# Optimization experiments

Measured on AMD Instinct MI355X. Metric: run time of the kernel, lower is better.

## Reference

```python
import jax, jax.numpy as jnp
import numpy as np

NUM, K = 5, 3  # grid intervals and spline order, as in KANLayer(num=5, k=3)

def _grid(num=NUM, k=K, lo=-1.0, hi=1.0):
    # base grid: num+1 points on [lo,hi], extended by k knots on each side (pykan extend_grid)
    h = (hi - lo) / num
    return jnp.linspace(lo - k * h, hi + k * h, num + 1 + 2 * k, dtype=jnp.float32)

def b_spline_basis(x, grid, k=K):
    # Cox-de Boor recursion, identical to pykan B_batch. x: (B, In) -> (B, In, num+k)
    xe = x[..., None]
    b = ((xe >= grid[:-1]) & (xe < grid[1:])).astype(x.dtype)  # order-0 indicators
    for d in range(1, k + 1):
        left = (xe - grid[:-(d + 1)]) / (grid[d:-1] - grid[:-(d + 1)])
        right = (grid[d + 1:] - xe) / (grid[d + 1:] - grid[1:-d])
        b = left * b[..., :-1] + right * b[..., 1:]
    return b

def kan_layer(x, coef, sb, ssp, grid):
    # x: (B, In); coef: (Out, In, nb); sb/ssp: (Out, In). mask == 1.
    basis = b_spline_basis(x, grid)                       # (B, In, nb)
    spline = jnp.einsum('big,oig->boi', basis, coef)      # per-edge spline value
    y = sb[None] * jax.nn.silu(x)[:, None, :] + ssp[None] * spline  # (B, Out, In)
    return y.sum(axis=2)                                  # (B, Out)

def setup_inputs() -> dict:
    key = jax.random.key(0)
    ks = jax.random.split(key, 3)
    B, IN, H, OUT, NB = 128, 3072, 256, 10, NUM + K
    return {
        "x": jax.random.normal(ks[0], (B, IN), jnp.float32),
        "coef1": 0.1 * jax.random.normal(ks[1], (H, IN, NB), jnp.float32),
        "scale_base1": jnp.ones((H, IN), jnp.float32),
        "scale_sp1": jnp.ones((H, IN), jnp.float32),
        "coef2": 0.1 * jax.random.normal(ks[2], (OUT, H, NB), jnp.float32),
        "scale_base2": jnp.ones((OUT, H), jnp.float32),
        "scale_sp2": jnp.ones((OUT, H), jnp.float32),
    }

def reference(x, coef1, scale_base1, scale_sp1, coef2, scale_base2, scale_sp2):
    g = _grid()
    h = kan_layer(x, coef1, scale_base1, scale_sp1, g)
    h = jax.nn.selu(h)
    return kan_layer(h, coef2, scale_base2, scale_sp2, g)
```

## Files before the change

kernel.cpp:

```cpp
#include <hip/hip_runtime.h>
#include <hip/hip_bf16.h>
#include <math.h>


#define B_DIM   128
#define IN1     3072
#define OUT1    256
#define NB      8
#define OUT2    10

#define KTOT    27648
#define ROWB    55296
#define SPLITK  108
#define BN      64

typedef short  bf16x8 __attribute__((ext_vector_type(8)));
typedef float  f32x4  __attribute__((ext_vector_type(4)));
typedef unsigned short ushort_t;
typedef unsigned int u32;

__device__ __forceinline__ ushort_t f2bf(float f) {
    union { __hip_bfloat16 h; ushort_t u; } v;
    v.h = __float2bfloat16(f);
    return v.u;
}
__device__ __forceinline__ float bf2f(ushort_t h) {
    union { float f; u32 u; } v; v.u = ((u32)h) << 16;
    return v.f;
}

__device__ __forceinline__ void gl_lds16(const void* g, void* l) {
    __builtin_amdgcn_global_load_lds(
        (const __attribute__((address_space(1))) u32*)g,
        (__attribute__((address_space(3))) u32*)l, 16, 0, 0);
}

__device__ __forceinline__ void basis_silu(float x, float w[8], float& sil) {
    sil = x / (1.0f + __expf(-x));
    float u  = (x + 2.2f) * 2.5f;
    float uf = floorf(u);
    int   j  = (int)uf;
    float t  = u - uf;
    float omt = 1.0f - t;
    float t2 = t * t, t3 = t2 * t;
    float w0 = omt * omt * omt * (1.0f / 6.0f);
    float w1 = (3.0f * t3 - 6.0f * t2 + 4.0f) * (1.0f / 6.0f);
    float w2 = (-3.0f * t3 + 3.0f * t2 + 3.0f * t + 1.0f) * (1.0f / 6.0f);
    float w3 = t3 * (1.0f / 6.0f);
    bool valid = (u >= 0.0f) && (u < 11.0f);
#pragma unroll
    for (int g = 0; g < 8; ++g) {
        int m = g - j + 3;
        float v = (m == 0) ? w0 : (m == 1) ? w1 : (m == 2) ? w2 : (m == 3) ? w3 : 0.0f;
        w[g] = valid ? v : 0.0f;
    }
}

__device__ __forceinline__ float selu_f(float x) {
    const float scale = 1.0507009873554805f;
    const float alpha = 1.6732632423543772f;
    return (x > 0.0f) ? scale * x : scale * alpha * (__expf(x) - 1.0f);
}

__global__ __launch_bounds__(128) void kconv(const float* __restrict__ x,
                                             const float* __restrict__ coef1,
                                             const float* __restrict__ sb1,
                                             const float* __restrict__ ssp1,
                                             char* __restrict__ Ag,
                                             char* __restrict__ Wg) {
    const int blk = blockIdx.x;
    if (blk < 384) {
        const int gid = blk * 128 + threadIdx.x;
        const int b  = gid / 384;
        const int ig = gid - b * 384;
        const int i0 = ig * 8;

        float4 x0 = *reinterpret_cast<const float4*>(x + (size_t)b * IN1 + i0);
        float4 x1 = *reinterpret_cast<const float4*>(x + (size_t)b * IN1 + i0 + 4);
        float xa[8] = {x0.x, x0.y, x0.z, x0.w, x1.x, x1.y, x1.z, x1.w};

        float bs[8][8], sil[8];
#pragma unroll
        for (int p = 0; p < 8; ++p) basis_silu(xa[p], bs[p], sil[p]);

        char* rowp = Ag + (size_t)b * ROWB;
        const int qsw = ((ig & 7) ^ (b & 7)) << 4;
#pragma unroll
        for (int s = 0; s < 9; ++s) {
            ushort_t v[8];
#pragma unroll
            for (int p = 0; p < 8; ++p)
                v[p] = f2bf((s < 8) ? bs[p][s] : sil[p]);
            *reinterpret_cast<uint4*>(rowp + (s * 48 + (ig >> 3)) * 128 + qsw) =
                *reinterpret_cast<const uint4*>(v);
        }
    } else {
        const int gid = (blk - 384) * 128 + threadIdx.x;
        const int o  = gid / 384;
        const int ig = gid - o * 384;
        const int i0 = ig * 8;

        float cf[8][8], sspv[8], sbv[8];
#pragma unroll
        for (int p = 0; p < 8; ++p) {
            const float* cp = coef1 + ((size_t)o * IN1 + i0 + p) * NB;
            float4 c0 = *reinterpret_cast<const float4*>(cp);
            float4 c1 = *reinterpret_cast<const float4*>(cp + 4);
            cf[p][0] = c0.x; cf[p][1] = c0.y; cf[p][2] = c0.z; cf[p][3] = c0.w;
            cf[p][4] = c1.x; cf[p][5] = c1.y; cf[p][6] = c1.z; cf[p][7] = c1.w;
        }
        {
            float4 s0 = *reinterpret_cast<const float4*>(ssp1 + (size_t)o * IN1 + i0);
            float4 s1 = *reinterpret_cast<const float4*>(ssp1 + (size_t)o * IN1 + i0 + 4);
            sspv[0]=s0.x; sspv[1]=s0.y; sspv[2]=s0.z; sspv[3]=s0.w;
            sspv[4]=s1.x; sspv[5]=s1.y; sspv[6]=s1.z; sspv[7]=s1.w;
            float4 b0 = *reinterpret_cast<const float4*>(sb1 + (size_t)o * IN1 + i0);
            float4 b1 = *reinterpret_cast<const float4*>(sb1 + (size_t)o * IN1 + i0 + 4);
            sbv[0]=b0.x; sbv[1]=b0.y; sbv[2]=b0.z; sbv[3]=b0.w;
            sbv[4]=b1.x; sbv[5]=b1.y; sbv[6]=b1.z; sbv[7]=b1.w;
        }

        char* rowp = Wg + (size_t)o * ROWB;
        const int qsw = ((ig & 7) ^ (o & 7)) << 4;
#pragma unroll
        for (int s = 0; s < 9; ++s) {
            ushort_t v[8];
#pragma unroll
            for (int p = 0; p < 8; ++p)
                v[p] = f2bf((s < 8) ? cf[p][s] * sspv[p] : sbv[p]);
            *reinterpret_cast<uint4*>(rowp + (s * 48 + (ig >> 3)) * 128 + qsw) =
                *reinterpret_cast<const uint4*>(v);
        }
    }
}

__global__ __launch_bounds__(512) void kgemm(const char* __restrict__ Ag,
                                             const char* __restrict__ Wg,
                                             ushort_t* __restrict__ partial) {
    __shared__ __align__(16) char lds[2][24576];

    const int tid = threadIdx.x;
    const int w   = tid >> 6, l = tid & 63;
    const int nt  = blockIdx.x, kc = blockIdx.y;
    const int o0  = nt * BN;

    const int ar0 = tid >> 3;
    const int ar1 = 64 + (tid >> 3);
    const int aq  = tid & 7;
    const char* Asrc0 = Ag + (size_t)ar0 * ROWB + ((aq ^ (ar0 & 7)) << 4);
    const char* Asrc1 = Ag + (size_t)ar1 * ROWB + ((aq ^ (ar1 & 7)) << 4);
    const int wr = tid >> 3;
    const char* Wsrc = Wg + (size_t)(o0 + wr) * ROWB + ((aq ^ (wr & 7)) << 4);

#define ISSUE(ss, buf)                                                        \
    {                                                                         \
        const int cb = (kc * 4 + (ss)) * 128;                                 \
        char* base = &lds[buf][0];                                            \
        gl_lds16(Asrc0 + cb, base + w * 1024);                                \
        gl_lds16(Asrc1 + cb, base + 8192 + w * 1024);                         \
        gl_lds16(Wsrc  + cb, base + 16384 + w * 1024);                        \
    }

    f32x4 acc[2][2];
#pragma unroll
    for (int a = 0; a < 2; ++a)
#pragma unroll
        for (int bq = 0; bq < 2; ++bq) acc[a][bq] = (f32x4){0.f, 0.f, 0.f, 0.f};

    const int mq = w >> 1, nq = w & 1;
    const int r16 = l & 15, k16 = l >> 4;

    ISSUE(0, 0)
    ISSUE(1, 1)

#pragma unroll
    for (int s = 0; s < 4; ++s) {
        if (s < 3) { asm volatile("s_waitcnt vmcnt(3)" ::: "memory"); }
        else       { asm volatile("s_waitcnt vmcnt(0)" ::: "memory"); }
        __builtin_amdgcn_s_barrier();
        asm volatile("" ::: "memory");

        const char* Ab = &lds[s & 1][0];
        const char* Wb = &lds[s & 1][16384];
#pragma unroll
        for (int ks = 0; ks < 2; ++ks) {
            const int qf = ks * 4 + k16;
            bf16x8 bf[2], af[2];
#pragma unroll
            for (int bq = 0; bq < 2; ++bq) {
                const int rn = nq * 32 + bq * 16 + r16;
                bf[bq] = *reinterpret_cast<const bf16x8*>(Wb + rn * 128 + ((qf ^ (rn & 7)) << 4));
            }
#pragma unroll
            for (int a = 0; a < 2; ++a) {
                const int rm = mq * 32 + a * 16 + r16;
                af[a] = *reinterpret_cast<const bf16x8*>(Ab + rm * 128 + ((qf ^ (rm & 7)) << 4));
            }
#pragma unroll
            for (int a = 0; a < 2; ++a)
#pragma unroll
                for (int bq = 0; bq < 2; ++bq)
                    acc[a][bq] = __builtin_amdgcn_mfma_f32_16x16x32_bf16(af[a], bf[bq], acc[a][bq], 0, 0, 0);
        }

        __builtin_amdgcn_s_barrier();
        asm volatile("" ::: "memory");
        if (s == 0) ISSUE(2, 0)
        if (s == 1) ISSUE(3, 1)
    }
#undef ISSUE

    ushort_t* pp = partial + (size_t)kc * (B_DIM * OUT1);
#pragma unroll
    for (int a = 0; a < 2; ++a) {
#pragma unroll
        for (int bq = 0; bq < 2; ++bq) {
            const int col = o0 + nq * 32 + bq * 16 + r16;
#pragma unroll
            for (int r = 0; r < 4; ++r) {
                const int row = mq * 32 + a * 16 + k16 * 4 + r;
                pp[(size_t)row * OUT1 + col] = f2bf(acc[a][bq][r]);
            }
        }
    }
}

__global__ __launch_bounds__(256) void klayer2r(const ushort_t* __restrict__ partial,
                                                const float* __restrict__ coef2,
                                                const float* __restrict__ sb2,
                                                const float* __restrict__ ssp2,
                                                float* __restrict__ out) {
    const int b = blockIdx.x;
    const int t = threadIdx.x;
    const int w = t >> 6, l = t & 63;

    f32x4 s = {0.f, 0.f, 0.f, 0.f};
    const ushort_t* pb = partial + (size_t)b * OUT1 + l * 4;
#pragma unroll
    for (int c = 0; c < 27; ++c) {
        ushort4 v = *reinterpret_cast<const ushort4*>(
            pb + (size_t)(w + 4 * c) * (B_DIM * OUT1));
        s[0] += bf2f(v.x); s[1] += bf2f(v.y); s[2] += bf2f(v.z); s[3] += bf2f(v.w);
    }

    __shared__ float sums[4][OUT1];
    *reinterpret_cast<float4*>(&sums[w][l * 4]) = (float4){s[0], s[1], s[2], s[3]};
    __syncthreads();

    const float hv = sums[0][t] + sums[1][t] + sums[2][t] + sums[3][t];
    const float sh = selu_f(hv);
    float w8[8], sil;
    basis_silu(sh, w8, sil);

    float accs[OUT2];
#pragma unroll
    for (int oo = 0; oo < OUT2; ++oo) {
        const float* cp = coef2 + ((size_t)oo * OUT1 + t) * NB;
        float4 c0 = *reinterpret_cast<const float4*>(cp);
        float4 c1 = *reinterpret_cast<const float4*>(cp + 4);
        float dot = w8[0] * c0.x + w8[1] * c0.y + w8[2] * c0.z + w8[3] * c0.w +
                    w8[4] * c1.x + w8[5] * c1.y + w8[6] * c1.z + w8[7] * c1.w;
        accs[oo] = sb2[oo * OUT1 + t] * sil + ssp2[oo * OUT1 + t] * dot;
    }

    __shared__ float red[4][OUT2];
#pragma unroll
    for (int oo = 0; oo < OUT2; ++oo) {
        float v = accs[oo];
#pragma unroll
        for (int off = 32; off >= 1; off >>= 1) v += __shfl_xor(v, off, 64);
        if (l == 0) red[w][oo] = v;
    }
    __syncthreads();
    if (t < OUT2)
        out[b * OUT2 + t] = red[0][t] + red[1][t] + red[2][t] + red[3][t];
}

extern "C" void kernel_launch(void* const* d_in, const int* in_sizes, int n_in,
                              void* d_out, int out_size, void* d_ws, size_t ws_size,
                              hipStream_t stream) {
    const float* x     = (const float*)d_in[0];
    const float* coef1 = (const float*)d_in[1];
    const float* sb1   = (const float*)d_in[2];
    const float* ssp1  = (const float*)d_in[3];
    const float* coef2 = (const float*)d_in[4];
    const float* sb2   = (const float*)d_in[5];
    const float* ssp2  = (const float*)d_in[6];
    float* out = (float*)d_out;

    char*     Ag      = (char*)d_ws;
    char*     Wg      = Ag + (size_t)B_DIM * ROWB;
    ushort_t* partial = (ushort_t*)(Wg + (size_t)OUT1 * ROWB);

    kconv<<<1152, 128, 0, stream>>>(x, coef1, sb1, ssp1, Ag, Wg);
    kgemm<<<dim3(OUT1 / BN, SPLITK), 512, 0, stream>>>(Ag, Wg, partial);
    klayer2r<<<B_DIM, 256, 0, stream>>>(partial, coef2, sb2, ssp2, out);
}
```

Measured before the change: 36.27 us.

## Split conversion kernel and stage through LDS for coalesced loads and stores

Result: slower. 38.11 us (+5.1%).

```diff
diff --git a/kernel.cpp b/kernel.cpp
--- a/kernel.cpp
+++ b/kernel.cpp
@@ -62,74 +62,89 @@
     return (x > 0.0f) ? scale * x : scale * alpha * (__expf(x) - 1.0f);
 }
 
-__global__ __launch_bounds__(128) void kconv(const float* __restrict__ x,
-                                             const float* __restrict__ coef1,
-                                             const float* __restrict__ sb1,
-                                             const float* __restrict__ ssp1,
-                                             char* __restrict__ Ag,
-                                             char* __restrict__ Wg) {
-    const int blk = blockIdx.x;
-    if (blk < 384) {
-        const int gid = blk * 128 + threadIdx.x;
-        const int b  = gid / 384;
-        const int ig = gid - b * 384;
-        const int i0 = ig * 8;
-
-        float4 x0 = *reinterpret_cast<const float4*>(x + (size_t)b * IN1 + i0);
-        float4 x1 = *reinterpret_cast<const float4*>(x + (size_t)b * IN1 + i0 + 4);
-        float xa[8] = {x0.x, x0.y, x0.z, x0.w, x1.x, x1.y, x1.z, x1.w};
-
-        float bs[8][8], sil[8];
-#pragma unroll
-        for (int p = 0; p < 8; ++p) basis_silu(xa[p], bs[p], sil[p]);
-
-        char* rowp = Ag + (size_t)b * ROWB;
-        const int qsw = ((ig & 7) ^ (b & 7)) << 4;
-#pragma unroll
-        for (int s = 0; s < 9; ++s) {
-            ushort_t v[8];
-#pragma unroll
-            for (int p = 0; p < 8; ++p)
-                v[p] = f2bf((s < 8) ? bs[p][s] : sil[p]);
-            *reinterpret_cast<uint4*>(rowp + (s * 48 + (ig >> 3)) * 128 + qsw) =
-                *reinterpret_cast<const uint4*>(v);
-        }
-    } else {
-        const int gid = (blk - 384) * 128 + threadIdx.x;
-        const int o  = gid / 384;
-        const int ig = gid - o * 384;
-        const int i0 = ig * 8;
-
-        float cf[8][8], sspv[8], sbv[8];
-#pragma unroll
-        for (int p = 0; p < 8; ++p) {
-            const float* cp = coef1 + ((size_t)o * IN1 + i0 + p) * NB;
-            float4 c0 = *reinterpret_cast<const float4*>(cp);
-            float4 c1 = *reinterpret_cast<const float4*>(cp + 4);
-            cf[p][0] = c0.x; cf[p][1] = c0.y; cf[p][2] = c0.z; cf[p][3] = c0.w;
-            cf[p][4] = c1.x; cf[p][5] = c1.y; cf[p][6] = c1.z; cf[p][7] = c1.w;
-        }
-        {
-            float4 s0 = *reinterpret_cast<const float4*>(ssp1 + (size_t)o * IN1 + i0);
-            float4 s1 = *reinterpret_cast<const float4*>(ssp1 + (size_t)o * IN1 + i0 + 4);
-            sspv[0]=s0.x; sspv[1]=s0.y; sspv[2]=s0.z; sspv[3]=s0.w;
-            sspv[4]=s1.x; sspv[5]=s1.y; sspv[6]=s1.z; sspv[7]=s1.w;
-            float4 b0 = *reinterpret_cast<const float4*>(sb1 + (size_t)o * IN1 + i0);
-            float4 b1 = *reinterpret_cast<const float4*>(sb1 + (size_t)o * IN1 + i0 + 4);
-            sbv[0]=b0.x; sbv[1]=b0.y; sbv[2]=b0.z; sbv[3]=b0.w;
-            sbv[4]=b1.x; sbv[5]=b1.y; sbv[6]=b1.z; sbv[7]=b1.w;
-        }
-
-        char* rowp = Wg + (size_t)o * ROWB;
-        const int qsw = ((ig & 7) ^ (o & 7)) << 4;
-#pragma unroll
-        for (int s = 0; s < 9; ++s) {
-            ushort_t v[8];
-#pragma unroll
-            for (int p = 0; p < 8; ++p)
-                v[p] = f2bf((s < 8) ? cf[p][s] * sspv[p] : sbv[p]);
-            *reinterpret_cast<uint4*>(rowp + (s * 48 + (ig >> 3)) * 128 + qsw) =
-                *reinterpret_cast<const uint4*>(v);
+#define APAD 8
+__global__ __launch_bounds__(256) void kconv_a(const float* __restrict__ x,
+                                               char* __restrict__ Ag) {
+    __shared__ ushort_t lds[9][1024 + APAD];
+    const int tid = threadIdx.x;
+    const int b  = blockIdx.x / 3;
+    const int i0 = (blockIdx.x % 3) * 1024;
+
+    {
+        const int li = tid * 4;
+        float4 xv = *reinterpret_cast<const float4*>(x + (size_t)b * IN1 + i0 + li);
+        float xa[4] = {xv.x, xv.y, xv.z, xv.w};
+#pragma unroll
+        for (int p = 0; p < 4; ++p) {
+            float bs[8], sil;
+            basis_silu(xa[p], bs, sil);
+#pragma unroll
+            for (int s = 0; s < 8; ++s) lds[s][li + p] = f2bf(bs[s]);
+            lds[8][li + p] = f2bf(sil);
+        }
+    }
+    __syncthreads();
+
+    char* rowp = Ag + (size_t)b * ROWB;
+    const int bsw = b & 7;
+#pragma unroll
+    for (int r = 0; r < 5; ++r) {
+        const int u = tid + r * 256;
+        if (u < 1152) {
+            const int s = u >> 7, q = u & 127;
+            const int ig = (i0 >> 3) + q;
+            uint4 v = *reinterpret_cast<const uint4*>(&lds[s][q * 8]);
+            *reinterpret_cast<uint4*>(rowp + (s * 48 + (ig >> 3)) * 128 +
+                                      (((ig & 7) ^ bsw) << 4)) = v;
+        }
+    }
+}
+
+#define WPAD 16
+__global__ __launch_bounds__(256) void kconv_w(const float* __restrict__ coef1,
+                                               const float* __restrict__ sb1,
+                                               const float* __restrict__ ssp1,
+                                               char* __restrict__ Wg) {
+    __shared__ ushort_t lds[9][512 + WPAD];
+    const int tid = threadIdx.x;
+    const int o  = blockIdx.x / 6;
+    const int i0 = (blockIdx.x % 6) * 512;
+
+    {
+        const int li = tid * 2;
+        const size_t e = (size_t)o * IN1 + i0 + li;
+        const float* cp = coef1 + e * NB;
+        float4 c0 = *reinterpret_cast<const float4*>(cp);
+        float4 c1 = *reinterpret_cast<const float4*>(cp + 4);
+        float4 c2 = *reinterpret_cast<const float4*>(cp + 8);
+        float4 c3 = *reinterpret_cast<const float4*>(cp + 12);
+        float2 sspv = *reinterpret_cast<const float2*>(ssp1 + e);
+        float2 sbv  = *reinterpret_cast<const float2*>(sb1 + e);
+
+        lds[0][li] = f2bf(c0.x * sspv.x); lds[1][li] = f2bf(c0.y * sspv.x);
+        lds[2][li] = f2bf(c0.z * sspv.x); lds[3][li] = f2bf(c0.w * sspv.x);
+        lds[4][li] = f2bf(c1.x * sspv.x); lds[5][li] = f2bf(c1.y * sspv.x);
+        lds[6][li] = f2bf(c1.z * sspv.x); lds[7][li] = f2bf(c1.w * sspv.x);
+        lds[8][li] = f2bf(sbv.x);
+        lds[0][li+1] = f2bf(c2.x * sspv.y); lds[1][li+1] = f2bf(c2.y * sspv.y);
+        lds[2][li+1] = f2bf(c2.z * sspv.y); lds[3][li+1] = f2bf(c2.w * sspv.y);
+        lds[4][li+1] = f2bf(c3.x * sspv.y); lds[5][li+1] = f2bf(c3.y * sspv.y);
+        lds[6][li+1] = f2bf(c3.z * sspv.y); lds[7][li+1] = f2bf(c3.w * sspv.y);
+        lds[8][li+1] = f2bf(sbv.y);
+    }
+    __syncthreads();
+
+    char* rowp = Wg + (size_t)o * ROWB;
+    const int osw = o & 7;
+#pragma unroll
+    for (int r = 0; r < 3; ++r) {
+        const int u = tid + r * 256;
+        if (u < 576) {
+            const int s = u >> 6, q = u & 63;
+            const int ig = (i0 >> 3) + q;
+            uint4 v = *reinterpret_cast<const uint4*>(&lds[s][q * 8]);
+            *reinterpret_cast<uint4*>(rowp + (s * 48 + (ig >> 3)) * 128 +
+                                      (((ig & 7) ^ osw) << 4)) = v;
         }
     }
 }
@@ -225,7 +240,7 @@
     }
 }
 
-__global__ __launch_bounds__(256) void klayer2r(const ushort_t* __restrict__ partial,
+__global__ __launch_bounds__(512) void klayer2r(const ushort_t* __restrict__ partial,
                                                 const float* __restrict__ coef2,
                                                 const float* __restrict__ sb2,
                                                 const float* __restrict__ ssp2,
@@ -233,43 +248,50 @@
     const int b = blockIdx.x;
     const int t = threadIdx.x;
     const int w = t >> 6, l = t & 63;
+    __shared__ float sums[8][OUT1];
+    __shared__ float red[4][OUT2];
 
     f32x4 s = {0.f, 0.f, 0.f, 0.f};
     const ushort_t* pb = partial + (size_t)b * OUT1 + l * 4;
 #pragma unroll
-    for (int c = 0; c < 27; ++c) {
+    for (int c = 0; c < 13; ++c) {
         ushort4 v = *reinterpret_cast<const ushort4*>(
-            pb + (size_t)(w + 4 * c) * (B_DIM * OUT1));
+            pb + (size_t)(w + 8 * c) * (B_DIM * OUT1));
         s[0] += bf2f(v.x); s[1] += bf2f(v.y); s[2] += bf2f(v.z); s[3] += bf2f(v.w);
     }
-
-    __shared__ float sums[4][OUT1];
+    if (w < 4) {
+        ushort4 v = *reinterpret_cast<const ushort4*>(
+            pb + (size_t)(w + 104) * (B_DIM * OUT1));
+        s[0] += bf2f(v.x); s[1] += bf2f(v.y); s[2] += bf2f(v.z); s[3] += bf2f(v.w);
+    }
     *reinterpret_cast<float4*>(&sums[w][l * 4]) = (float4){s[0], s[1], s[2], s[3]};
     __syncthreads();
 
-    const float hv = sums[0][t] + sums[1][t] + sums[2][t] + sums[3][t];
-    const float sh = selu_f(hv);
-    float w8[8], sil;
-    basis_silu(sh, w8, sil);
-
-    float accs[OUT2];
-#pragma unroll
-    for (int oo = 0; oo < OUT2; ++oo) {
-        const float* cp = coef2 + ((size_t)oo * OUT1 + t) * NB;
-        float4 c0 = *reinterpret_cast<const float4*>(cp);
-        float4 c1 = *reinterpret_cast<const float4*>(cp + 4);
-        float dot = w8[0] * c0.x + w8[1] * c0.y + w8[2] * c0.z + w8[3] * c0.w +
-                    w8[4] * c1.x + w8[5] * c1.y + w8[6] * c1.z + w8[7] * c1.w;
-        accs[oo] = sb2[oo * OUT1 + t] * sil + ssp2[oo * OUT1 + t] * dot;
-    }
-
-    __shared__ float red[4][OUT2];
-#pragma unroll
-    for (int oo = 0; oo < OUT2; ++oo) {
-        float v = accs[oo];
-#pragma unroll
-        for (int off = 32; off >= 1; off >>= 1) v += __shfl_xor(v, off, 64);
-        if (l == 0) red[w][oo] = v;
+    if (t < OUT1) {
+        const float hv = sums[0][t] + sums[1][t] + sums[2][t] + sums[3][t] +
+                         sums[4][t] + sums[5][t] + sums[6][t] + sums[7][t];
+        const float sh = selu_f(hv);
+        float w8[8], sil;
+        basis_silu(sh, w8, sil);
+
+        float accs[OUT2];
+#pragma unroll
+        for (int oo = 0; oo < OUT2; ++oo) {
+            const float* cp = coef2 + ((size_t)oo * OUT1 + t) * NB;
+            float4 c0 = *reinterpret_cast<const float4*>(cp);
+            float4 c1 = *reinterpret_cast<const float4*>(cp + 4);
+            float dot = w8[0] * c0.x + w8[1] * c0.y + w8[2] * c0.z + w8[3] * c0.w +
+                        w8[4] * c1.x + w8[5] * c1.y + w8[6] * c1.z + w8[7] * c1.w;
+            accs[oo] = sb2[oo * OUT1 + t] * sil + ssp2[oo * OUT1 + t] * dot;
+        }
+
+#pragma unroll
+        for (int oo = 0; oo < OUT2; ++oo) {
+            float v = accs[oo];
+#pragma unroll
+            for (int off = 32; off >= 1; off >>= 1) v += __shfl_xor(v, off, 64);
+            if (l == 0) red[w][oo] = v;
+        }
     }
     __syncthreads();
     if (t < OUT2)
@@ -292,7 +314,8 @@
     char*     Wg      = Ag + (size_t)B_DIM * ROWB;
     ushort_t* partial = (ushort_t*)(Wg + (size_t)OUT1 * ROWB);
 
-    kconv<<<1152, 128, 0, stream>>>(x, coef1, sb1, ssp1, Ag, Wg);
+    kconv_a<<<384, 256, 0, stream>>>(x, Ag);
+    kconv_w<<<1536, 256, 0, stream>>>(coef1, sb1, ssp1, Wg);
     kgemm<<<dim3(OUT1 / BN, SPLITK), 512, 0, stream>>>(Ag, Wg, partial);
-    klayer2r<<<B_DIM, 256, 0, stream>>>(partial, coef2, sb2, ssp2, out);
-}
+    klayer2r<<<B_DIM, 512, 0, stream>>>(partial, coef2, sb2, ssp2, out);
+}
```

## Fuse basis construction and weight scaling into the split-K GEMM

Applied to the files above, without the earlier changes.

Measured after the change: 41.03 us. 13.1% more time.

```diff
diff --git a/kernel.cpp b/kernel.cpp
--- a/kernel.cpp
+++ b/kernel.cpp
@@ -9,9 +9,7 @@
 #define NB      8
 #define OUT2    10
 
-#define KTOT    27648
-#define ROWB    55296
-#define SPLITK  108
+#define SPLITK  96
 #define BN      64
 
 typedef short  bf16x8 __attribute__((ext_vector_type(8)));
@@ -33,6 +31,14 @@
     __builtin_amdgcn_global_load_lds(
         (const __attribute__((address_space(1))) u32*)g,
         (__attribute__((address_space(3))) u32*)l, 16, 0, 0);
+}
+
+__device__ __forceinline__ bf16x8 pack8(float a0, float a1, float a2, float a3,
+                                        float a4, float a5, float a6, float a7) {
+    union { ushort_t u[8]; bf16x8 v; } r;
+    r.u[0] = f2bf(a0); r.u[1] = f2bf(a1); r.u[2] = f2bf(a2); r.u[3] = f2bf(a3);
+    r.u[4] = f2bf(a4); r.u[5] = f2bf(a5); r.u[6] = f2bf(a6); r.u[7] = f2bf(a7);
+    return r.v;
 }
 
 __device__ __forceinline__ void basis_silu(float x, float w[8], float& sil) {
@@ -62,153 +68,153 @@
     return (x > 0.0f) ? scale * x : scale * alpha * (__expf(x) - 1.0f);
 }
 
-__global__ __launch_bounds__(128) void kconv(const float* __restrict__ x,
-                                             const float* __restrict__ coef1,
-                                             const float* __restrict__ sb1,
-                                             const float* __restrict__ ssp1,
-                                             char* __restrict__ Ag,
-                                             char* __restrict__ Wg) {
-    const int blk = blockIdx.x;
-    if (blk < 384) {
-        const int gid = blk * 128 + threadIdx.x;
-        const int b  = gid / 384;
-        const int ig = gid - b * 384;
-        const int i0 = ig * 8;
-
-        float4 x0 = *reinterpret_cast<const float4*>(x + (size_t)b * IN1 + i0);
-        float4 x1 = *reinterpret_cast<const float4*>(x + (size_t)b * IN1 + i0 + 4);
-        float xa[8] = {x0.x, x0.y, x0.z, x0.w, x1.x, x1.y, x1.z, x1.w};
-
-        float bs[8][8], sil[8];
-#pragma unroll
-        for (int p = 0; p < 8; ++p) basis_silu(xa[p], bs[p], sil[p]);
-
-        char* rowp = Ag + (size_t)b * ROWB;
-        const int qsw = ((ig & 7) ^ (b & 7)) << 4;
-#pragma unroll
-        for (int s = 0; s < 9; ++s) {
-            ushort_t v[8];
-#pragma unroll
-            for (int p = 0; p < 8; ++p)
-                v[p] = f2bf((s < 8) ? bs[p][s] : sil[p]);
-            *reinterpret_cast<uint4*>(rowp + (s * 48 + (ig >> 3)) * 128 + qsw) =
-                *reinterpret_cast<const uint4*>(v);
-        }
-    } else {
-        const int gid = (blk - 384) * 128 + threadIdx.x;
-        const int o  = gid / 384;
-        const int ig = gid - o * 384;
-        const int i0 = ig * 8;
-
-        float cf[8][8], sspv[8], sbv[8];
-#pragma unroll
-        for (int p = 0; p < 8; ++p) {
-            const float* cp = coef1 + ((size_t)o * IN1 + i0 + p) * NB;
-            float4 c0 = *reinterpret_cast<const float4*>(cp);
-            float4 c1 = *reinterpret_cast<const float4*>(cp + 4);
-            cf[p][0] = c0.x; cf[p][1] = c0.y; cf[p][2] = c0.z; cf[p][3] = c0.w;
-            cf[p][4] = c1.x; cf[p][5] = c1.y; cf[p][6] = c1.z; cf[p][7] = c1.w;
-        }
-        {
-            float4 s0 = *reinterpret_cast<const float4*>(ssp1 + (size_t)o * IN1 + i0);
-            float4 s1 = *reinterpret_cast<const float4*>(ssp1 + (size_t)o * IN1 + i0 + 4);
-            sspv[0]=s0.x; sspv[1]=s0.y; sspv[2]=s0.z; sspv[3]=s0.w;
-            sspv[4]=s1.x; sspv[5]=s1.y; sspv[6]=s1.z; sspv[7]=s1.w;
-            float4 b0 = *reinterpret_cast<const float4*>(sb1 + (size_t)o * IN1 + i0);
-            float4 b1 = *reinterpret_cast<const float4*>(sb1 + (size_t)o * IN1 + i0 + 4);
-            sbv[0]=b0.x; sbv[1]=b0.y; sbv[2]=b0.z; sbv[3]=b0.w;
-            sbv[4]=b1.x; sbv[5]=b1.y; sbv[6]=b1.z; sbv[7]=b1.w;
-        }
-
-        char* rowp = Wg + (size_t)o * ROWB;
-        const int qsw = ((ig & 7) ^ (o & 7)) << 4;
-#pragma unroll
-        for (int s = 0; s < 9; ++s) {
-            ushort_t v[8];
-#pragma unroll
-            for (int p = 0; p < 8; ++p)
-                v[p] = f2bf((s < 8) ? cf[p][s] * sspv[p] : sbv[p]);
-            *reinterpret_cast<uint4*>(rowp + (s * 48 + (ig >> 3)) * 128 + qsw) =
-                *reinterpret_cast<const uint4*>(v);
-        }
-    }
-}
-
-__global__ __launch_bounds__(512) void kgemm(const char* __restrict__ Ag,
-                                             const char* __restrict__ Wg,
-                                             ushort_t* __restrict__ partial) {
-    __shared__ __align__(16) char lds[2][24576];
+__global__ __launch_bounds__(256) void ktranspose(const float* __restrict__ x,
+                                                  float* __restrict__ xT) {
+    __shared__ float t[32][33];
+    int bx = blockIdx.x, by = blockIdx.y;
+    int tx = threadIdx.x, ty = threadIdx.y;
+#pragma unroll
+    for (int k = 0; k < 4; ++k)
+        t[ty + k * 8][tx] = x[(by * 32 + ty + k * 8) * IN1 + bx * 32 + tx];
+    __syncthreads();
+#pragma unroll
+    for (int k = 0; k < 4; ++k)
+        xT[(bx * 32 + ty + k * 8) * B_DIM + by * 32 + tx] = t[tx][ty + k * 8];
+}
+
+__global__ __launch_bounds__(512, 2) void kgemm_fused(
+        const float* __restrict__ xT,
+        const float* __restrict__ coef1,
+        const float* __restrict__ sb1,
+        const float* __restrict__ ssp1,
+        ushort_t* __restrict__ partial) {
+    __shared__ __align__(16) char smem[65024];
+    char* Ab0 = smem;
+    char* Ab1 = smem + 10240;
+    char* Wb0 = smem + 20480;
+    char* Wb1 = smem + 28672;
+    char* silb = smem + 36864;
+    char* sspb = smem + 47104;
+    char* sbb  = smem + 55808;
 
     const int tid = threadIdx.x;
-    const int w   = tid >> 6, l = tid & 63;
-    const int nt  = blockIdx.x, kc = blockIdx.y;
+    const int w = tid >> 6, l = tid & 63;
+    const int nt = blockIdx.x, kc = blockIdx.y;
     const int o0  = nt * BN;
-
-    const int ar0 = tid >> 3;
-    const int ar1 = 64 + (tid >> 3);
-    const int aq  = tid & 7;
-    const char* Asrc0 = Ag + (size_t)ar0 * ROWB + ((aq ^ (ar0 & 7)) << 4);
-    const char* Asrc1 = Ag + (size_t)ar1 * ROWB + ((aq ^ (ar1 & 7)) << 4);
-    const int wr = tid >> 3;
-    const char* Wsrc = Wg + (size_t)(o0 + wr) * ROWB + ((aq ^ (wr & 7)) << 4);
-
-#define ISSUE(ss, buf)                                                        \
-    {                                                                         \
-        const int cb = (kc * 4 + (ss)) * 128;                                 \
-        char* base = &lds[buf][0];                                            \
-        gl_lds16(Asrc0 + cb, base + w * 1024);                                \
-        gl_lds16(Asrc1 + cb, base + 8192 + w * 1024);                         \
-        gl_lds16(Wsrc  + cb, base + 16384 + w * 1024);                        \
-    }
-
-    f32x4 acc[2][2];
-#pragma unroll
-    for (int a = 0; a < 2; ++a)
-#pragma unroll
-        for (int bq = 0; bq < 2; ++bq) acc[a][bq] = (f32x4){0.f, 0.f, 0.f, 0.f};
-
+    const int i0c = kc * 32;
     const int mq = w >> 1, nq = w & 1;
     const int r16 = l & 15, k16 = l >> 4;
 
-    ISSUE(0, 0)
-    ISSUE(1, 1)
-
-#pragma unroll
-    for (int s = 0; s < 4; ++s) {
-        if (s < 3) { asm volatile("s_waitcnt vmcnt(3)" ::: "memory"); }
-        else       { asm volatile("s_waitcnt vmcnt(0)" ::: "memory"); }
-        __builtin_amdgcn_s_barrier();
-        asm volatile("" ::: "memory");
-
-        const char* Ab = &lds[s & 1][0];
-        const char* Wb = &lds[s & 1][16384];
-#pragma unroll
-        for (int ks = 0; ks < 2; ++ks) {
-            const int qf = ks * 4 + k16;
-            bf16x8 bf[2], af[2];
+    const int ab  = tid & 127;
+    const int ail = tid >> 7;
+    const int wo  = tid >> 3;
+    const int wul = (tid & 7) ^ (wo & 7);
+
+#define WISSUE(ss, Wdst)                                                       \
+    {                                                                          \
+        const float* gsrc = coef1 +                                            \
+            ((size_t)(o0 + wo) * IN1 + (i0c + (ss) * 4 + (wul >> 1))) * 8 +    \
+            (wul & 1) * 4;                                                     \
+        gl_lds16(gsrc, (Wdst) + w * 1024);                                     \
+    }
+
+#define ACOMPUTE(ss, Adst)                                                     \
+    {                                                                          \
+        float xv = xT[(size_t)(i0c + (ss) * 4 + ail) * B_DIM + ab];            \
+        float bs[8], sil;                                                      \
+        basis_silu(xv, bs, sil);                                               \
+        ushort_t v[8];                                                         \
+        v[0]=f2bf(bs[0]); v[1]=f2bf(bs[1]); v[2]=f2bf(bs[2]); v[3]=f2bf(bs[3]);\
+        v[4]=f2bf(bs[4]); v[5]=f2bf(bs[5]); v[6]=f2bf(bs[6]); v[7]=f2bf(bs[7]);\
+        *reinterpret_cast<uint4*>((Adst) + ab * 80 + ail * 16) =               \
+            *reinterpret_cast<const uint4*>(v);                                \
+        *reinterpret_cast<ushort_t*>(silb + ab * 80 + ((ss) * 4 + ail) * 2) =  \
+            f2bf(sil);                                                         \
+    }
+
+    f32x4 acc[2][2];
+#pragma unroll
+    for (int a = 0; a < 2; ++a)
+#pragma unroll
+        for (int bq = 0; bq < 2; ++bq) acc[a][bq] = (f32x4){0.f, 0.f, 0.f, 0.f};
+
+    WISSUE(0, Wb0)
+    {
+        const int o = tid >> 3, iw = tid & 7;
+        const size_t e = (size_t)(o0 + o) * IN1 + i0c + iw * 4;
+        float4 sv = *reinterpret_cast<const float4*>(ssp1 + e);
+        *reinterpret_cast<float2*>(sspb + o * 136 + iw * 16)     = (float2){sv.x, sv.y};
+        *reinterpret_cast<float2*>(sspb + o * 136 + iw * 16 + 8) = (float2){sv.z, sv.w};
+        float4 bv = *reinterpret_cast<const float4*>(sb1 + e);
+        *reinterpret_cast<float4*>(sbb + o * 144 + iw * 16) = bv;
+    }
+    ACOMPUTE(0, Ab0)
+    asm volatile("s_waitcnt vmcnt(0)" ::: "memory");
+    __syncthreads();
+
+#pragma unroll 1
+    for (int s = 0; s < 8; ++s) {
+        char* Acur = (s & 1) ? Ab1 : Ab0;
+        char* Wcur = (s & 1) ? Wb1 : Wb0;
+        char* Anxt = (s & 1) ? Ab0 : Ab1;
+        char* Wnxt = (s & 1) ? Wb0 : Wb1;
+
+        if (s < 7) {
+            WISSUE(s + 1, Wnxt)
+            ACOMPUTE(s + 1, Anxt)
+        }
+
+        {
+            bf16x8 bfr[2], af[2];
 #pragma unroll
             for (int bq = 0; bq < 2; ++bq) {
-                const int rn = nq * 32 + bq * 16 + r16;
-                bf[bq] = *reinterpret_cast<const bf16x8*>(Wb + rn * 128 + ((qf ^ (rn & 7)) << 4));
+                const int ol = nq * 32 + bq * 16 + r16;
+                const int u0 = (k16 * 2)     ^ (ol & 7);
+                const int u1 = (k16 * 2 + 1) ^ (ol & 7);
+                f32x4 wa = *reinterpret_cast<const f32x4*>(Wcur + ol * 128 + u0 * 16);
+                f32x4 wb = *reinterpret_cast<const f32x4*>(Wcur + ol * 128 + u1 * 16);
+                float sv = *reinterpret_cast<const float*>(sspb + ol * 136 + (s * 4 + k16) * 4);
+                bfr[bq] = pack8(wa[0] * sv, wa[1] * sv, wa[2] * sv, wa[3] * sv,
+                                wb[0] * sv, wb[1] * sv, wb[2] * sv, wb[3] * sv);
             }
 #pragma unroll
             for (int a = 0; a < 2; ++a) {
                 const int rm = mq * 32 + a * 16 + r16;
-                af[a] = *reinterpret_cast<const bf16x8*>(Ab + rm * 128 + ((qf ^ (rm & 7)) << 4));
+                af[a] = *reinterpret_cast<const bf16x8*>(Acur + rm * 80 + k16 * 16);
             }
 #pragma unroll
             for (int a = 0; a < 2; ++a)
 #pragma unroll
                 for (int bq = 0; bq < 2; ++bq)
-                    acc[a][bq] = __builtin_amdgcn_mfma_f32_16x16x32_bf16(af[a], bf[bq], acc[a][bq], 0, 0, 0);
-        }
-
-        __builtin_amdgcn_s_barrier();
-        asm volatile("" ::: "memory");
-        if (s == 0) ISSUE(2, 0)
-        if (s == 1) ISSUE(3, 1)
-    }
-#undef ISSUE
+                    acc[a][bq] = __builtin_amdgcn_mfma_f32_16x16x32_bf16(af[a], bfr[bq], acc[a][bq], 0, 0, 0);
+        }
+
+        if (s < 7) {
+            asm volatile("s_waitcnt vmcnt(0)" ::: "memory");
+            __syncthreads();
+        }
+    }
+
+    {
+        bf16x8 bfr[2], af[2];
+#pragma unroll
+        for (int bq = 0; bq < 2; ++bq) {
+            const int ol = nq * 32 + bq * 16 + r16;
+            f32x4 s0 = *reinterpret_cast<const f32x4*>(sbb + ol * 144 + k16 * 32);
+            f32x4 s1 = *reinterpret_cast<const f32x4*>(sbb + ol * 144 + k16 * 32 + 16);
+            bfr[bq] = pack8(s0[0], s0[1], s0[2], s0[3], s1[0], s1[1], s1[2], s1[3]);
+        }
+#pragma unroll
+        for (int a = 0; a < 2; ++a) {
+            const int rm = mq * 32 + a * 16 + r16;
+            af[a] = *reinterpret_cast<const bf16x8*>(silb + rm * 80 + k16 * 16);
+        }
+#pragma unroll
+        for (int a = 0; a < 2; ++a)
+#pragma unroll
+            for (int bq = 0; bq < 2; ++bq)
+                acc[a][bq] = __builtin_amdgcn_mfma_f32_16x16x32_bf16(af[a], bfr[bq], acc[a][bq], 0, 0, 0);
+    }
 
     ushort_t* pp = partial + (size_t)kc * (B_DIM * OUT1);
 #pragma unroll
@@ -223,9 +229,11 @@
             }
         }
     }
-}
-
-__global__ __launch_bounds__(256) void klayer2r(const ushort_t* __restrict__ partial,
+#undef WISSUE
+#undef ACOMPUTE
+}
+
+__global__ __launch_bounds__(512) void klayer2r(const ushort_t* __restrict__ partial,
                                                 const float* __restrict__ coef2,
                                                 const float* __restrict__ sb2,
                                                 const float* __restrict__ ssp2,
@@ -233,43 +241,46 @@
     const int b = blockIdx.x;
     const int t = threadIdx.x;
     const int w = t >> 6, l = t & 63;
+    __shared__ float sums[8][OUT1];
+    __shared__ float red[4][OUT2];
 
     f32x4 s = {0.f, 0.f, 0.f, 0.f};
     const ushort_t* pb = partial + (size_t)b * OUT1 + l * 4;
 #pragma unroll
-    for (int c = 0; c < 27; ++c) {
+    for (int c = 0; c < 12; ++c) {
         ushort4 v = *reinterpret_cast<const ushort4*>(
-            pb + (size_t)(w + 4 * c) * (B_DIM * OUT1));
+            pb + (size_t)(w + 8 * c) * (B_DIM * OUT1));
         s[0] += bf2f(v.x); s[1] += bf2f(v.y); s[2] += bf2f(v.z); s[3] += bf2f(v.w);
     }
-
-    __shared__ float sums[4][OUT1];
     *reinterpret_cast<float4*>(&sums[w][l * 4]) = (float4){s[0], s[1], s[2], s[3]};
     __syncthreads();
 
-    const float hv = sums[0][t] + sums[1][t] + sums[2][t] + sums[3][t];
-    const float sh = selu_f(hv);
-    float w8[8], sil;
-    basis_silu(sh, w8, sil);
-
-    float accs[OUT2];
-#pragma unroll
-    for (int oo = 0; oo < OUT2; ++oo) {
-        const float* cp = coef2 + ((size_t)oo * OUT1 + t) * NB;
-        float4 c0 = *reinterpret_cast<const float4*>(cp);
-        float4 c1 = *reinterpret_cast<const float4*>(cp + 4);
-        float dot = w8[0] * c0.x + w8[1] * c0.y + w8[2] * c0.z + w8[3] * c0.w +
-                    w8[4] * c1.x + w8[5] * c1.y + w8[6] * c1.z + w8[7] * c1.w;
-        accs[oo] = sb2[oo * OUT1 + t] * sil + ssp2[oo * OUT1 + t] * dot;
-    }
-
-    __shared__ float red[4][OUT2];
-#pragma unroll
-    for (int oo = 0; oo < OUT2; ++oo) {
-        float v = accs[oo];
-#pragma unroll
-        for (int off = 32; off >= 1; off >>= 1) v += __shfl_xor(v, off, 64);
-        if (l == 0) red[w][oo] = v;
+    if (t < OUT1) {
+        float hv = 0.0f;
+#pragma unroll
+        for (int ww = 0; ww < 8; ++ww) hv += sums[ww][t];
+        const float sh = selu_f(hv);
+        float w8[8], sil;
+        basis_silu(sh, w8, sil);
+
+        float accs[OUT2];
+#pragma unroll
+        for (int oo = 0; oo < OUT2; ++oo) {
+            const float* cp = coef2 + ((size_t)oo * OUT1 + t) * NB;
+            float4 c0 = *reinterpret_cast<const float4*>(cp);
+            float4 c1 = *reinterpret_cast<const float4*>(cp + 4);
+            float dot = w8[0] * c0.x + w8[1] * c0.y + w8[2] * c0.z + w8[3] * c0.w +
+                        w8[4] * c1.x + w8[5] * c1.y + w8[6] * c1.z + w8[7] * c1.w;
+            accs[oo] = sb2[oo * OUT1 + t] * sil + ssp2[oo * OUT1 + t] * dot;
+        }
+
+#pragma unroll
+        for (int oo = 0; oo < OUT2; ++oo) {
+            float v = accs[oo];
+#pragma unroll
+            for (int off = 32; off >= 1; off >>= 1) v += __shfl_xor(v, off, 64);
+            if (l == 0) red[w][oo] = v;
+        }
     }
     __syncthreads();
     if (t < OUT2)
@@ -288,11 +299,10 @@
     const float* ssp2  = (const float*)d_in[6];
     float* out = (float*)d_out;
 
-    char*     Ag      = (char*)d_ws;
-    char*     Wg      = Ag + (size_t)B_DIM * ROWB;
-    ushort_t* partial = (ushort_t*)(Wg + (size_t)OUT1 * ROWB);
-
-    kconv<<<1152, 128, 0, stream>>>(x, coef1, sb1, ssp1, Ag, Wg);
-    kgemm<<<dim3(OUT1 / BN, SPLITK), 512, 0, stream>>>(Ag, Wg, partial);
-    klayer2r<<<B_DIM, 256, 0, stream>>>(partial, coef2, sb2, ssp2, out);
-}
+    float*    xT      = (float*)d_ws;
+    ushort_t* partial = (ushort_t*)((char*)d_ws + 1572864);
+
+    ktranspose<<<dim3(96, 4), dim3(32, 8), 0, stream>>>(x, xT);
+    kgemm_fused<<<dim3(OUT1 / BN, SPLITK), 512, 0, stream>>>(xT, coef1, sb1, ssp1, partial);
+    klayer2r<<<B_DIM, 512, 0, stream>>>(partial, coef2, sb2, ssp2, out);
+}
```
